# Kernel optimization log

Hardware: AMD Instinct MI355X
Metric: run time of the kernel (lower is better)

The kernel has to match this reference:

```python
import jax, jax.numpy as jnp
import numpy as np

# Standard FP4 E2M1 lookup table (nvfp4-style): sign bit in nibble MSB.
FP4_LUT = jnp.array([0.0, 0.5, 1.0, 1.5, 2.0, 3.0, 4.0, 6.0,
                     -0.0, -0.5, -1.0, -1.5, -2.0, -3.0, -4.0, -6.0],
                    dtype=jnp.float32)


def dequant_fp4(packed_i32, scales, group_size):
    """packed_i32: [K/8, N] int32 (8 fp4 nibbles per word, low nibble first);
    scales: [K/group_size, N]. Returns dense fp32 weight [K, N]."""
    w = jax.lax.bitcast_convert_type(packed_i32, jnp.uint32)  # [K/8, N]
    # Unpack nibbles along the reduction axis: nibble i -> row 8*r + i.
    nib = jnp.stack([(w >> jnp.uint32(4 * i)) & jnp.uint32(0xF) for i in range(8)],
                    axis=1)                                    # [K/8, 8, N]
    K = nib.shape[0] * 8
    nib = nib.reshape(K, w.shape[1])                           # [K, N]
    vals = FP4_LUT[nib]                                        # [K, N]
    s = jnp.repeat(scales, group_size, axis=0)                 # [K, N]
    return vals * s


def setup_inputs() -> dict:
    key = jax.random.key(0)
    k1, k2, k3, k4, k5, k6 = jax.random.split(key, 6)
    tokens, H, I, G = 4096, 2048, 5632, 128
    return {
        "hidden": jax.random.normal(k1, (tokens, H), dtype=jnp.float32),
        "moe_output": jax.random.normal(k2, (tokens, H), dtype=jnp.float32),
        "gate_up_weights": jax.random.randint(k3, (H // 8, 2 * I), 0, 2147483647, dtype=jnp.int32),
        "gate_up_scales": jax.random.uniform(k4, (H // G, 2 * I), dtype=jnp.float32, minval=0.01, maxval=0.1),
        "down_weights": jax.random.randint(k5, (I // 8, H), 0, 2147483647, dtype=jnp.int32),
        "down_scales": jax.random.uniform(k6, (I // G, H), dtype=jnp.float32, minval=0.01, maxval=0.1),
        "group_size": G,
    }


def reference(hidden, moe_output, gate_up_weights, gate_up_scales,
              down_weights, down_scales, group_size):
    # Shared-expert SwiGLU FFN with FP4 group-quantized weights, fused residual add.
    W_gu = dequant_fp4(gate_up_weights, gate_up_scales, group_size)  # [H, 2I]
    gu = hidden @ W_gu                                               # [T, 2I]
    I = gu.shape[1] // 2
    gate, up = gu[:, :I], gu[:, I:]
    act = jax.nn.silu(gate) * up                                     # [T, I]
    W_d = dequant_fp4(down_weights, down_scales, group_size)         # [I, H]
    return moe_output + act @ W_d                                    # [T, H]
```

## Files before the change

### kernel.cpp

```cpp
#include <hip/hip_runtime.h>
#include <hip/hip_fp16.h>
#include <stdint.h>

#define TOKENS 4096
#define HDIM   2048
#define IDIM   5632
#define BM 128
#define BN 128
#define BK 64

#define G1_NP  11264
#define G1_KSB (G1_NP * 64)
#define G2_KSB (HDIM * 64)

typedef _Float16 f16x8 __attribute__((ext_vector_type(8)));
typedef float    f32x4 __attribute__((ext_vector_type(4)));

__device__ __forceinline__ uint32_t dec2(uint32_t z, uint32_t s2u) {
    uint32_t sgn = (z << 12) & 0x80008000u;
    uint32_t h   = ((z << 9) & 0x0E000E00u) | sgn;
    __half2 hv = __builtin_bit_cast(__half2, h);
    __half2 sv = __builtin_bit_cast(__half2, s2u);
    __half2 r  = __hmul2(hv, sv);
    return __builtin_bit_cast(uint32_t, r);
}
__device__ __forceinline__ int4 dec8(uint32_t w, uint32_t s2u) {
    int4 d;
    d.x = (int)dec2( w        & 0x000F000Fu, s2u);
    d.y = (int)dec2((w >> 4)  & 0x000F000Fu, s2u);
    d.z = (int)dec2((w >> 8)  & 0x000F000Fu, s2u);
    d.w = (int)dec2((w >> 12) & 0x000F000Fu, s2u);
    return d;
}
__device__ __forceinline__ uint32_t scale_s2u(float sc) {
    uint16_t hs = __builtin_bit_cast(uint16_t, __float2half(sc * 16384.0f));
    return (uint32_t)hs * 0x00010001u;
}
__device__ __forceinline__ uint32_t packh(float lo, float hi) {
    __half2 h2 = __halves2half2(__float2half(lo), __float2half(hi));
    return __builtin_bit_cast(uint32_t, h2);
}
__device__ __forceinline__ void gl_lds16(const void* g, void* l) {
    __builtin_amdgcn_global_load_lds(
        (const __attribute__((address_space(1))) uint32_t*)g,
        (__attribute__((address_space(3))) uint32_t*)l, 16, 0, 0);
}

__global__ __launch_bounds__(256) void convert_hidden(
    const float* __restrict__ src, __half* __restrict__ dst)
{
    int idx = blockIdx.x * 256 + threadIdx.x;
    const float4* s = (const float4*)src + (size_t)idx * 2;
    float4 a = s[0], b = s[1];
    int4 v;
    v.x = (int)packh(a.x, b.x);
    v.y = (int)packh(a.y, b.y);
    v.z = (int)packh(a.z, b.z);
    v.w = (int)packh(a.w, b.w);
    *((int4*)dst + idx) = v;
}

__global__ __launch_bounds__(256) void dequant_wgu5(
    const uint32_t* __restrict__ W, const float* __restrict__ S,
    __half* __restrict__ Bt)
{
    __shared__ __half L[256 * 64];
    const int kt = blockIdx.y;
    const int t  = threadIdx.x;
    const int np = blockIdx.x * 256 + t;
    const int sc = (np >> 6) * 32 + (np & 31) + (((np >> 5) & 1) ? IDIM : 0);
    uint32_t s2u = scale_s2u(S[(size_t)(kt >> 1) * (2 * IDIM) + sc]);
    #pragma unroll
    for (int j = 0; j < 8; ++j) {
        uint32_t w = W[(size_t)(kt * 8 + j) * (2 * IDIM) + sc];
        int4 d = dec8(w, s2u);
        *(int4*)&L[t * 64 + ((j ^ (t & 7)) << 3)] = d;
    }
    __syncthreads();
    __half* dst = Bt + (size_t)kt * G1_KSB + (size_t)blockIdx.x * 256 * 64;
    #pragma unroll
    for (int k = 0; k < 8; ++k) {
        int c = k * 256 + t;
        int row = c >> 3, s = c & 7;
        int4 d = *(const int4*)&L[row * 64 + ((s ^ (row & 7)) << 3)];
        *(int4*)(dst + c * 8) = d;
    }
}

__global__ __launch_bounds__(256) void dequant_wd5(
    const uint32_t* __restrict__ W, const float* __restrict__ S,
    __half* __restrict__ Bt)
{
    __shared__ __half L[256 * 64];
    const int kt = blockIdx.y;
    const int t  = threadIdx.x;
    const int n  = blockIdx.x * 256 + t;
    uint32_t s2u = scale_s2u(S[(size_t)(kt >> 1) * HDIM + n]);
    #pragma unroll
    for (int j = 0; j < 8; ++j) {
        uint32_t w = W[(size_t)(kt * 8 + j) * HDIM + n];
        int4 d = dec8(w, s2u);
        *(int4*)&L[t * 64 + ((j ^ (t & 7)) << 3)] = d;
    }
    __syncthreads();
    __half* dst = Bt + (size_t)kt * G2_KSB + (size_t)blockIdx.x * 256 * 64;
    #pragma unroll
    for (int k = 0; k < 8; ++k) {
        int c = k * 256 + t;
        int row = c >> 3, s = c & 7;
        int4 d = *(const int4*)&L[row * 64 + ((s ^ (row & 7)) << 3)];
        *(int4*)(dst + c * 8) = d;
    }
}

__global__ __launch_bounds__(256, 4) void gemm1_s(
    const __half* __restrict__ A, const __half* __restrict__ Bt,
    __half* __restrict__ act)
{
    __shared__ __half Alds[BM * 64];
    __shared__ __half Blds[BN * 64];
    const int tid  = threadIdx.x;
    const int lane = tid & 63;
    const int wid  = tid >> 6;
    const int wm = wid >> 1, wn = wid & 1;
    const int m0 = blockIdx.y * BM;
    const int n0 = blockIdx.x * BN;

    f32x4 acc[4][4];
    #pragma unroll
    for (int i = 0; i < 4; ++i)
        #pragma unroll
        for (int j = 0; j < 4; ++j) acc[i][j] = f32x4{0.f, 0.f, 0.f, 0.f};

    const __half* srcA[4];
    const __half* srcB[4];
    #pragma unroll
    for (int i = 0; i < 4; ++i) {
        int u = i * 256 + tid, row = u >> 3, s = u & 7, sl = s ^ (row & 7);
        srcA[i] = A  + (size_t)(m0 + row) * HDIM + sl * 8;
        srcB[i] = Bt + (size_t)(n0 + row) * 64 + sl * 8;
    }

    int aoff[4][2], boff[4][2];
    #pragma unroll
    for (int f = 0; f < 4; ++f)
        #pragma unroll
        for (int ks = 0; ks < 2; ++ks) {
            int kb = ks * 4 + (lane >> 4);
            int ra = wm * 64 + f * 16 + (lane & 15);
            int rb = wn * 64 + f * 16 + (lane & 15);
            aoff[f][ks] = ra * 128 + ((kb ^ (ra & 7)) << 4);
            boff[f][ks] = rb * 128 + ((kb ^ (rb & 7)) << 4);
        }

    for (int kt = 0; kt < HDIM / 64; ++kt) {
        #pragma unroll
        for (int i = 0; i < 4; ++i) {
            int u = i * 256 + tid;
            gl_lds16(srcA[i], (char*)Alds + u * 16);
            gl_lds16(srcB[i], (char*)Blds + u * 16);
            srcA[i] += 64;
            srcB[i] += G1_KSB;
        }
        __syncthreads();
        #pragma unroll
        for (int ks = 0; ks < 2; ++ks) {
            f16x8 af[4], bf[4];
            #pragma unroll
            for (int f = 0; f < 4; ++f) {
                af[f] = *(const f16x8*)((const char*)Alds + aoff[f][ks]);
                bf[f] = *(const f16x8*)((const char*)Blds + boff[f][ks]);
            }
            #pragma unroll
            for (int mi = 0; mi < 4; ++mi)
                #pragma unroll
                for (int ni = 0; ni < 4; ++ni)
                    acc[mi][ni] = __builtin_amdgcn_mfma_f32_16x16x32_f16(af[mi], bf[ni], acc[mi][ni], 0, 0, 0);
        }
        __syncthreads();
    }

    const int pairbase = ((n0 + wn * 64) >> 6) * 32;
    #pragma unroll
    for (int mi = 0; mi < 4; ++mi) {
        #pragma unroll
        for (int q = 0; q < 2; ++q) {
            int gcol = pairbase + q * 16 + (lane & 15);
            int colstore = (gcol & ~7) | (((gcol & 3) << 1) | ((gcol >> 2) & 1));
            #pragma unroll
            for (int r = 0; r < 4; ++r) {
                int m = m0 + wm * 64 + mi * 16 + (lane >> 4) * 4 + r;
                float gv = acc[mi][q][r];
                float uv = acc[mi][q + 2][r];
                float sig = 1.0f / (1.0f + __expf(-gv));
                act[(size_t)m * IDIM + colstore] = __float2half(gv * sig * uv);
            }
        }
    }
}

__global__ __launch_bounds__(256, 4) void gemm2_s(
    const __half* __restrict__ A, const __half* __restrict__ Bt,
    const float* __restrict__ moe, float* __restrict__ out)
{
    __shared__ __half Alds[BM * 64];
    __shared__ __half Blds[BN * 64];
    const int tid  = threadIdx.x;
    const int lane = tid & 63;
    const int wid  = tid >> 6;
    const int wm = wid >> 1, wn = wid & 1;
    const int m0 = blockIdx.y * BM;
    const int n0 = blockIdx.x * BN;

    f32x4 acc[4][4];
    #pragma unroll
    for (int i = 0; i < 4; ++i)
        #pragma unroll
        for (int j = 0; j < 4; ++j) acc[i][j] = f32x4{0.f, 0.f, 0.f, 0.f};

    const __half* srcA[4];
    const __half* srcB[4];
    #pragma unroll
    for (int i = 0; i < 4; ++i) {
        int u = i * 256 + tid, row = u >> 3, s = u & 7, sl = s ^ (row & 7);
        srcA[i] = A  + (size_t)(m0 + row) * IDIM + sl * 8;
        srcB[i] = Bt + (size_t)(n0 + row) * 64 + sl * 8;
    }

    int aoff[4][2], boff[4][2];
    #pragma unroll
    for (int f = 0; f < 4; ++f)
        #pragma unroll
        for (int ks = 0; ks < 2; ++ks) {
            int kb = ks * 4 + (lane >> 4);
            int ra = wm * 64 + f * 16 + (lane & 15);
            int rb = wn * 64 + f * 16 + (lane & 15);
            aoff[f][ks] = ra * 128 + ((kb ^ (ra & 7)) << 4);
            boff[f][ks] = rb * 128 + ((kb ^ (rb & 7)) << 4);
        }

    for (int kt = 0; kt < IDIM / 64; ++kt) {
        #pragma unroll
        for (int i = 0; i < 4; ++i) {
            int u = i * 256 + tid;
            gl_lds16(srcA[i], (char*)Alds + u * 16);
            gl_lds16(srcB[i], (char*)Blds + u * 16);
            srcA[i] += 64;
            srcB[i] += G2_KSB;
        }
        __syncthreads();
        #pragma unroll
        for (int ks = 0; ks < 2; ++ks) {
            f16x8 af[4], bf[4];
            #pragma unroll
            for (int f = 0; f < 4; ++f) {
                af[f] = *(const f16x8*)((const char*)Alds + aoff[f][ks]);
                bf[f] = *(const f16x8*)((const char*)Blds + boff[f][ks]);
            }
            #pragma unroll
            for (int mi = 0; mi < 4; ++mi)
                #pragma unroll
                for (int ni = 0; ni < 4; ++ni)
                    acc[mi][ni] = __builtin_amdgcn_mfma_f32_16x16x32_f16(af[mi], bf[ni], acc[mi][ni], 0, 0, 0);
        }
        __syncthreads();
    }
    #pragma unroll
    for (int mi = 0; mi < 4; ++mi) {
        #pragma unroll
        for (int ni = 0; ni < 4; ++ni) {
            int n = n0 + wn * 64 + ni * 16 + (lane & 15);
            #pragma unroll
            for (int r = 0; r < 4; ++r) {
                int m = m0 + wm * 64 + mi * 16 + (lane >> 4) * 4 + r;
                out[(size_t)m * HDIM + n] = moe[(size_t)m * HDIM + n] + acc[mi][ni][r];
            }
        }
    }
}

__global__ __launch_bounds__(256, 2) void gemm1_silu(
    const __half* __restrict__ A, const uint32_t* __restrict__ W,
    const float* __restrict__ S, __half* __restrict__ act)
{
    __shared__ __half Alds[BM * BK];
    __shared__ __half Blds[2][BN * BK];
    const int tid  = threadIdx.x;
    const int lane = tid & 63;
    const int wid  = tid >> 6;
    const int wm = wid >> 1, wn = wid & 1;
    const int m0 = blockIdx.y * BM;
    const int c0 = blockIdx.x * BN;

    f32x4 accg[4][4], accu[4][4];
    #pragma unroll
    for (int i = 0; i < 4; ++i)
        #pragma unroll
        for (int j = 0; j < 4; ++j) {
            accg[i][j] = f32x4{0.f, 0.f, 0.f, 0.f};
            accu[i][j] = f32x4{0.f, 0.f, 0.f, 0.f};
        }

    const int c = tid & 127;
    const int rbase = (tid >> 7) * 4;

    for (int kt = 0; kt < HDIM / BK; ++kt) {
        const int k0 = kt * BK;
        #pragma unroll
        for (int i = 0; i < 4; ++i) {
            int u = tid + i * 256;
            int row = u >> 3, kb = u & 7;
            int4 v = *(const int4*)(A + (size_t)(m0 + row) * HDIM + k0 + kb * 8);
            *(int4*)((char*)Alds + row * 128 + ((kb ^ (row & 7)) << 4)) = v;
        }
        const int g = k0 >> 7;
        #pragma unroll
        for (int p = 0; p < 2; ++p) {
            const int ncol = (p ? IDIM : 0) + c0 + c;
            uint32_t s2u = scale_s2u(S[(size_t)g * (2 * IDIM) + ncol]);
            #pragma unroll
            for (int i = 0; i < 4; ++i) {
                int rl = rbase + i;
                uint32_t w = W[(size_t)(kt * 8 + rl) * (2 * IDIM) + ncol];
                int4 d = dec8(w, s2u);
                *(int4*)((char*)&Blds[p][0] + c * 128 + ((rl ^ (c & 7)) << 4)) = d;
            }
        }
        __syncthreads();
        #pragma unroll
        for (int ks = 0; ks < 2; ++ks) {
            f16x8 af[4], bg[4], bu[4];
            const int kb = ks * 4 + (lane >> 4);
            #pragma unroll
            for (int mi = 0; mi < 4; ++mi) {
                int m = wm * 64 + mi * 16 + (lane & 15);
                af[mi] = *(const f16x8*)((const char*)Alds + m * 128 + ((kb ^ (m & 7)) << 4));
            }
            #pragma unroll
            for (int ni = 0; ni < 4; ++ni) {
                int n = wn * 64 + ni * 16 + (lane & 15);
                bg[ni] = *(const f16x8*)((const char*)&Blds[0][0] + n * 128 + ((kb ^ (n & 7)) << 4));
                bu[ni] = *(const f16x8*)((const char*)&Blds[1][0] + n * 128 + ((kb ^ (n & 7)) << 4));
            }
            #pragma unroll
            for (int mi = 0; mi < 4; ++mi)
                #pragma unroll
                for (int ni = 0; ni < 4; ++ni) {
                    accg[mi][ni] = __builtin_amdgcn_mfma_f32_16x16x32_f16(af[mi], bg[ni], accg[mi][ni], 0, 0, 0);
                    accu[mi][ni] = __builtin_amdgcn_mfma_f32_16x16x32_f16(af[mi], bu[ni], accu[mi][ni], 0, 0, 0);
                }
        }
        __syncthreads();
    }
    #pragma unroll
    for (int mi = 0; mi < 4; ++mi) {
        #pragma unroll
        for (int ni = 0; ni < 4; ++ni) {
            int nlog = c0 + wn * 64 + ni * 16 + (lane & 15);
            int ncol = (nlog & ~7) | (((nlog & 3) << 1) | ((nlog >> 2) & 1));
            #pragma unroll
            for (int r = 0; r < 4; ++r) {
                int m = m0 + wm * 64 + mi * 16 + (lane >> 4) * 4 + r;
                float gv = accg[mi][ni][r];
                float uv = accu[mi][ni][r];
                float sig = 1.0f / (1.0f + __expf(-gv));
                act[(size_t)m * IDIM + ncol] = __float2half(gv * sig * uv);
            }
        }
    }
}

__global__ __launch_bounds__(256, 2) void gemm2_add(
    const __half* __restrict__ A, const uint32_t* __restrict__ W,
    const float* __restrict__ S, const float* __restrict__ moe,
    float* __restrict__ out)
{
    __shared__ __half Alds[BM * BK];
    __shared__ __half Blds[BN * BK];
    const int tid  = threadIdx.x;
    const int lane = tid & 63;
    const int wid  = tid >> 6;
    const int wm = wid >> 1, wn = wid & 1;
    const int m0 = blockIdx.y * BM;
    const int n0 = blockIdx.x * BN;

    f32x4 acc[4][4];
    #pragma unroll
    for (int i = 0; i < 4; ++i)
        #pragma unroll
        for (int j = 0; j < 4; ++j) acc[i][j] = f32x4{0.f, 0.f, 0.f, 0.f};

    const int c = tid & 127;
    const int rbase = (tid >> 7) * 4;

    int aoff[4][2], boff[4][2];
    #pragma unroll
    for (int f = 0; f < 4; ++f)
        #pragma unroll
        for (int ks = 0; ks < 2; ++ks) {
            int kb = ks * 4 + (lane >> 4);
            int ra = wm * 64 + f * 16 + (lane & 15);
            int rb = wn * 64 + f * 16 + (lane & 15);
            aoff[f][ks] = ra * 128 + ((kb ^ (ra & 7)) << 4);
            boff[f][ks] = rb * 128 + ((kb ^ (rb & 7)) << 4);
        }

    for (int kt = 0; kt < IDIM / BK; ++kt) {
        const int k0 = kt * BK;
        #pragma unroll
        for (int i = 0; i < 4; ++i) {
            int u = tid + i * 256;
            int row = u >> 3, kb = u & 7;
            int4 v = *(const int4*)(A + (size_t)(m0 + row) * IDIM + k0 + kb * 8);
            *(int4*)((char*)Alds + row * 128 + ((kb ^ (row & 7)) << 4)) = v;
        }
        {
            const int g = k0 >> 7;
            const int ncol = n0 + c;
            uint32_t s2u = scale_s2u(S[(size_t)g * HDIM + ncol]);
            #pragma unroll
            for (int i = 0; i < 4; ++i) {
                int rl = rbase + i;
                uint32_t w = W[(size_t)(kt * 8 + rl) * HDIM + ncol];
                int4 d = dec8(w, s2u);
                *(int4*)((char*)Blds + c * 128 + ((rl ^ (c & 7)) << 4)) = d;
            }
        }
        __syncthreads();
        #pragma unroll
        for (int ks = 0; ks < 2; ++ks) {
            f16x8 af[4], bf[4];
            #pragma unroll
            for (int f = 0; f < 4; ++f) {
                af[f] = *(const f16x8*)((const char*)Alds + aoff[f][ks]);
                bf[f] = *(const f16x8*)((const char*)Blds + boff[f][ks]);
            }
            #pragma unroll
            for (int mi = 0; mi < 4; ++mi)
                #pragma unroll
                for (int ni = 0; ni < 4; ++ni)
                    acc[mi][ni] = __builtin_amdgcn_mfma_f32_16x16x32_f16(af[mi], bf[ni], acc[mi][ni], 0, 0, 0);
        }
        __syncthreads();
    }
    #pragma unroll
    for (int mi = 0; mi < 4; ++mi) {
        #pragma unroll
        for (int ni = 0; ni < 4; ++ni) {
            int n = n0 + wn * 64 + ni * 16 + (lane & 15);
            #pragma unroll
            for (int r = 0; r < 4; ++r) {
                int m = m0 + wm * 64 + mi * 16 + (lane >> 4) * 4 + r;
                out[(size_t)m * HDIM + n] = moe[(size_t)m * HDIM + n] + acc[mi][ni][r];
            }
        }
    }
}

extern "C" void kernel_launch(void* const* d_in, const int* in_sizes, int n_in,
                              void* d_out, int out_size, void* d_ws, size_t ws_size,
                              hipStream_t stream) {
    const float*    hidden = (const float*)d_in[0];
    const float*    moe    = (const float*)d_in[1];
    const uint32_t* wgu    = (const uint32_t*)d_in[2];
    const float*    sgu    = (const float*)d_in[3];
    const uint32_t* wd     = (const uint32_t*)d_in[4];
    const float*    sd     = (const float*)d_in[5];
    float* out = (float*)d_out;

    const size_t sz_hidden = (size_t)TOKENS * HDIM * 2;
    const size_t sz_act    = (size_t)TOKENS * IDIM * 2;
    const size_t sz_wgu16  = (size_t)HDIM * 2 * IDIM * 2;
    const size_t sz_wd16   = (size_t)IDIM * HDIM * 2;

    __half* hidden_f16 = (__half*)d_ws;
    __half* act        = (__half*)((char*)d_ws + sz_hidden);
    __half* wgu16      = (__half*)((char*)d_ws + sz_hidden + sz_act);
    __half* wd16       = (__half*)((char*)d_ws + sz_hidden + sz_act + sz_wgu16);

    const size_t need_g1 = sz_hidden + sz_act + sz_wgu16;
    const size_t need_g2 = need_g1 + sz_wd16;

    convert_hidden<<<dim3(TOKENS * HDIM / 8 / 256), dim3(256), 0, stream>>>(hidden, hidden_f16);

    if (ws_size >= need_g1) {
        dequant_wgu5<<<dim3(G1_NP / 256, 32), dim3(256), 0, stream>>>(wgu, sgu, wgu16);
        gemm1_s<<<dim3(G1_NP / BN, TOKENS / BM), dim3(256), 0, stream>>>(hidden_f16, wgu16, act);
    } else {
        gemm1_silu<<<dim3(IDIM / BN, TOKENS / BM), dim3(256), 0, stream>>>(hidden_f16, wgu, sgu, act);
    }

    if (ws_size >= need_g2) {
        dequant_wd5<<<dim3(HDIM / 256, IDIM / 64), dim3(256), 0, stream>>>(wd, sd, wd16);
        gemm2_s<<<dim3(HDIM / BN, TOKENS / BM), dim3(256), 0, stream>>>(act, wd16, moe, out);
    } else {
        gemm2_add<<<dim3(HDIM / BN, TOKENS / BM), dim3(256), 0, stream>>>(act, wd, sd, moe, out);
    }
}
```

Baseline: 317.7 us.

## Pre-swizzle gate/up weights into MFMA fragment order and load B directly to registers

The gate/up dequant kernel now writes fp16 weights in the exact per-lane MFMA fragment order, so the first GEMM loads B fragments straight from global memory into registers instead of staging them through LDS. This removes half the LDS traffic and B-tile LDS reads in gemm1, at the cost of depending on cache hits for B reuse across M-blocks. Occupancy is lowered to 3 waves per SIMD to make room for the extra registers. The fallback gemm2_add path also inlines its LDS offset computation.

```diff
diff --git a/kernel.cpp b/kernel.cpp
--- a/kernel.cpp
+++ b/kernel.cpp
@@ -60,7 +60,7 @@
     *((int4*)dst + idx) = v;
 }
 
-__global__ __launch_bounds__(256) void dequant_wgu5(
+__global__ __launch_bounds__(256) void dequant_wgu6(
     const uint32_t* __restrict__ W, const float* __restrict__ S,
     __half* __restrict__ Bt)
 {
@@ -77,7 +77,34 @@
         *(int4*)&L[t * 64 + ((j ^ (t & 7)) << 3)] = d;
     }
     __syncthreads();
-    __half* dst = Bt + (size_t)kt * G1_KSB + (size_t)blockIdx.x * 256 * 64;
+    __half* dst = Bt + (size_t)kt * G1_KSB + (size_t)blockIdx.x * 16384;
+    #pragma unroll
+    for (int k = 0; k < 8; ++k) {
+        int c = k * 256 + t;
+        int row = ((c >> 7) << 4) + (c & 15);
+        int w   = (((c >> 6) & 1) << 2) + ((c >> 4) & 3);
+        int4 d = *(const int4*)&L[row * 64 + ((w ^ (row & 7)) << 3)];
+        *(int4*)(dst + (size_t)c * 8) = d;
+    }
+}
+
+__global__ __launch_bounds__(256) void dequant_wd5(
+    const uint32_t* __restrict__ W, const float* __restrict__ S,
+    __half* __restrict__ Bt)
+{
+    __shared__ __half L[256 * 64];
+    const int kt = blockIdx.y;
+    const int t  = threadIdx.x;
+    const int n  = blockIdx.x * 256 + t;
+    uint32_t s2u = scale_s2u(S[(size_t)(kt >> 1) * HDIM + n]);
+    #pragma unroll
+    for (int j = 0; j < 8; ++j) {
+        uint32_t w = W[(size_t)(kt * 8 + j) * HDIM + n];
+        int4 d = dec8(w, s2u);
+        *(int4*)&L[t * 64 + ((j ^ (t & 7)) << 3)] = d;
+    }
+    __syncthreads();
+    __half* dst = Bt + (size_t)kt * G2_KSB + (size_t)blockIdx.x * 256 * 64;
     #pragma unroll
     for (int k = 0; k < 8; ++k) {
         int c = k * 256 + t;
@@ -87,35 +114,94 @@
     }
 }
 
-__global__ __launch_bounds__(256) void dequant_wd5(
-    const uint32_t* __restrict__ W, const float* __restrict__ S,
-    __half* __restrict__ Bt)
-{
-    __shared__ __half L[256 * 64];
-    const int kt = blockIdx.y;
-    const int t  = threadIdx.x;
-    const int n  = blockIdx.x * 256 + t;
-    uint32_t s2u = scale_s2u(S[(size_t)(kt >> 1) * HDIM + n]);
-    #pragma unroll
-    for (int j = 0; j < 8; ++j) {
-        uint32_t w = W[(size_t)(kt * 8 + j) * HDIM + n];
-        int4 d = dec8(w, s2u);
-        *(int4*)&L[t * 64 + ((j ^ (t & 7)) << 3)] = d;
-    }
-    __syncthreads();
-    __half* dst = Bt + (size_t)kt * G2_KSB + (size_t)blockIdx.x * 256 * 64;
-    #pragma unroll
-    for (int k = 0; k < 8; ++k) {
-        int c = k * 256 + t;
-        int row = c >> 3, s = c & 7;
-        int4 d = *(const int4*)&L[row * 64 + ((s ^ (row & 7)) << 3)];
-        *(int4*)(dst + c * 8) = d;
-    }
-}
-
-__global__ __launch_bounds__(256, 4) void gemm1_s(
+__global__ __launch_bounds__(256, 3) void gemm1_f(
     const __half* __restrict__ A, const __half* __restrict__ Bt,
     __half* __restrict__ act)
+{
+    __shared__ __half Alds[BM * 64];
+    const int tid  = threadIdx.x;
+    const int lane = tid & 63;
+    const int wid  = tid >> 6;
+    const int wm = wid >> 1, wn = wid & 1;
+    const int m0 = blockIdx.y * BM;
+    const int n0 = blockIdx.x * BN;
+
+    f32x4 acc[4][4];
+    #pragma unroll
+    for (int i = 0; i < 4; ++i)
+        #pragma unroll
+        for (int j = 0; j < 4; ++j) acc[i][j] = f32x4{0.f, 0.f, 0.f, 0.f};
+
+    const __half* srcA[4];
+    #pragma unroll
+    for (int i = 0; i < 4; ++i) {
+        int u = i * 256 + tid, row = u >> 3, s = u & 7, sl = s ^ (row & 7);
+        srcA[i] = A + (size_t)(m0 + row) * HDIM + sl * 8;
+    }
+
+    const __half* pB = Bt + ((size_t)((n0 >> 4) + wn * 4) * 2) * 512 + lane * 8;
+
+    int aoff[4][2];
+    #pragma unroll
+    for (int f = 0; f < 4; ++f)
+        #pragma unroll
+        for (int ks = 0; ks < 2; ++ks) {
+            int kb = ks * 4 + (lane >> 4);
+            int ra = wm * 64 + f * 16 + (lane & 15);
+            aoff[f][ks] = ra * 128 + ((kb ^ (ra & 7)) << 4);
+        }
+
+    for (int kt = 0; kt < HDIM / 64; ++kt) {
+        f16x8 bf[4][2];
+        #pragma unroll
+        for (int ni = 0; ni < 4; ++ni)
+            #pragma unroll
+            for (int ks = 0; ks < 2; ++ks)
+                bf[ni][ks] = *(const f16x8*)(pB + (size_t)kt * G1_KSB + (ni * 2 + ks) * 512);
+        #pragma unroll
+        for (int i = 0; i < 4; ++i) {
+            int u = i * 256 + tid;
+            gl_lds16(srcA[i], (char*)Alds + u * 16);
+            srcA[i] += 64;
+        }
+        __syncthreads();
+        #pragma unroll
+        for (int ks = 0; ks < 2; ++ks) {
+            f16x8 af[4];
+            #pragma unroll
+            for (int f = 0; f < 4; ++f)
+                af[f] = *(const f16x8*)((const char*)Alds + aoff[f][ks]);
+            #pragma unroll
+            for (int mi = 0; mi < 4; ++mi)
+                #pragma unroll
+                for (int ni = 0; ni < 4; ++ni)
+                    acc[mi][ni] = __builtin_amdgcn_mfma_f32_16x16x32_f16(af[mi], bf[ni][ks], acc[mi][ni], 0, 0, 0);
+        }
+        __syncthreads();
+    }
+
+    const int pairbase = ((n0 + wn * 64) >> 6) * 32;
+    #pragma unroll
+    for (int mi = 0; mi < 4; ++mi) {
+        #pragma unroll
+        for (int q = 0; q < 2; ++q) {
+            int gcol = pairbase + q * 16 + (lane & 15);
+            int colstore = (gcol & ~7) | (((gcol & 3) << 1) | ((gcol >> 2) & 1));
+            #pragma unroll
+            for (int r = 0; r < 4; ++r) {
+                int m = m0 + wm * 64 + mi * 16 + (lane >> 4) * 4 + r;
+                float gv = acc[mi][q][r];
+                float uv = acc[mi][q + 2][r];
+                float sig = 1.0f / (1.0f + __expf(-gv));
+                act[(size_t)m * IDIM + colstore] = __float2half(gv * sig * uv);
+            }
+        }
+    }
+}
+
+__global__ __launch_bounds__(256, 4) void gemm2_s(
+    const __half* __restrict__ A, const __half* __restrict__ Bt,
+    const float* __restrict__ moe, float* __restrict__ out)
 {
     __shared__ __half Alds[BM * 64];
     __shared__ __half Blds[BN * 64];
@@ -137,92 +223,6 @@
     #pragma unroll
     for (int i = 0; i < 4; ++i) {
         int u = i * 256 + tid, row = u >> 3, s = u & 7, sl = s ^ (row & 7);
-        srcA[i] = A  + (size_t)(m0 + row) * HDIM + sl * 8;
-        srcB[i] = Bt + (size_t)(n0 + row) * 64 + sl * 8;
-    }
-
-    int aoff[4][2], boff[4][2];
-    #pragma unroll
-    for (int f = 0; f < 4; ++f)
-        #pragma unroll
-        for (int ks = 0; ks < 2; ++ks) {
-            int kb = ks * 4 + (lane >> 4);
-            int ra = wm * 64 + f * 16 + (lane & 15);
-            int rb = wn * 64 + f * 16 + (lane & 15);
-            aoff[f][ks] = ra * 128 + ((kb ^ (ra & 7)) << 4);
-            boff[f][ks] = rb * 128 + ((kb ^ (rb & 7)) << 4);
-        }
-
-    for (int kt = 0; kt < HDIM / 64; ++kt) {
-        #pragma unroll
-        for (int i = 0; i < 4; ++i) {
-            int u = i * 256 + tid;
-            gl_lds16(srcA[i], (char*)Alds + u * 16);
-            gl_lds16(srcB[i], (char*)Blds + u * 16);
-            srcA[i] += 64;
-            srcB[i] += G1_KSB;
-        }
-        __syncthreads();
-        #pragma unroll
-        for (int ks = 0; ks < 2; ++ks) {
-            f16x8 af[4], bf[4];
-            #pragma unroll
-            for (int f = 0; f < 4; ++f) {
-                af[f] = *(const f16x8*)((const char*)Alds + aoff[f][ks]);
-                bf[f] = *(const f16x8*)((const char*)Blds + boff[f][ks]);
-            }
-            #pragma unroll
-            for (int mi = 0; mi < 4; ++mi)
-                #pragma unroll
-                for (int ni = 0; ni < 4; ++ni)
-                    acc[mi][ni] = __builtin_amdgcn_mfma_f32_16x16x32_f16(af[mi], bf[ni], acc[mi][ni], 0, 0, 0);
-        }
-        __syncthreads();
-    }
-
-    const int pairbase = ((n0 + wn * 64) >> 6) * 32;
-    #pragma unroll
-    for (int mi = 0; mi < 4; ++mi) {
-        #pragma unroll
-        for (int q = 0; q < 2; ++q) {
-            int gcol = pairbase + q * 16 + (lane & 15);
-            int colstore = (gcol & ~7) | (((gcol & 3) << 1) | ((gcol >> 2) & 1));
-            #pragma unroll
-            for (int r = 0; r < 4; ++r) {
-                int m = m0 + wm * 64 + mi * 16 + (lane >> 4) * 4 + r;
-                float gv = acc[mi][q][r];
-                float uv = acc[mi][q + 2][r];
-                float sig = 1.0f / (1.0f + __expf(-gv));
-                act[(size_t)m * IDIM + colstore] = __float2half(gv * sig * uv);
-            }
-        }
-    }
-}
-
-__global__ __launch_bounds__(256, 4) void gemm2_s(
-    const __half* __restrict__ A, const __half* __restrict__ Bt,
-    const float* __restrict__ moe, float* __restrict__ out)
-{
-    __shared__ __half Alds[BM * 64];
-    __shared__ __half Blds[BN * 64];
-    const int tid  = threadIdx.x;
-    const int lane = tid & 63;
-    const int wid  = tid >> 6;
-    const int wm = wid >> 1, wn = wid & 1;
-    const int m0 = blockIdx.y * BM;
-    const int n0 = blockIdx.x * BN;
-
-    f32x4 acc[4][4];
-    #pragma unroll
-    for (int i = 0; i < 4; ++i)
-        #pragma unroll
-        for (int j = 0; j < 4; ++j) acc[i][j] = f32x4{0.f, 0.f, 0.f, 0.f};
-
-    const __half* srcA[4];
-    const __half* srcB[4];
-    #pragma unroll
-    for (int i = 0; i < 4; ++i) {
-        int u = i * 256 + tid, row = u >> 3, s = u & 7, sl = s ^ (row & 7);
         srcA[i] = A  + (size_t)(m0 + row) * IDIM + sl * 8;
         srcB[i] = Bt + (size_t)(n0 + row) * 64 + sl * 8;
     }
@@ -393,18 +393,6 @@
     const int c = tid & 127;
     const int rbase = (tid >> 7) * 4;
 
-    int aoff[4][2], boff[4][2];
-    #pragma unroll
-    for (int f = 0; f < 4; ++f)
-        #pragma unroll
-        for (int ks = 0; ks < 2; ++ks) {
-            int kb = ks * 4 + (lane >> 4);
-            int ra = wm * 64 + f * 16 + (lane & 15);
-            int rb = wn * 64 + f * 16 + (lane & 15);
-            aoff[f][ks] = ra * 128 + ((kb ^ (ra & 7)) << 4);
-            boff[f][ks] = rb * 128 + ((kb ^ (rb & 7)) << 4);
-        }
-
     for (int kt = 0; kt < IDIM / BK; ++kt) {
         const int k0 = kt * BK;
         #pragma unroll
@@ -430,10 +418,16 @@
         #pragma unroll
         for (int ks = 0; ks < 2; ++ks) {
             f16x8 af[4], bf[4];
-            #pragma unroll
-            for (int f = 0; f < 4; ++f) {
-                af[f] = *(const f16x8*)((const char*)Alds + aoff[f][ks]);
-                bf[f] = *(const f16x8*)((const char*)Blds + boff[f][ks]);
+            const int kb = ks * 4 + (lane >> 4);
+            #pragma unroll
+            for (int mi = 0; mi < 4; ++mi) {
+                int m = wm * 64 + mi * 16 + (lane & 15);
+                af[mi] = *(const f16x8*)((const char*)Alds + m * 128 + ((kb ^ (m & 7)) << 4));
+            }
+            #pragma unroll
+            for (int ni = 0; ni < 4; ++ni) {
+                int n = wn * 64 + ni * 16 + (lane & 15);
+                bf[ni] = *(const f16x8*)((const char*)Blds + n * 128 + ((kb ^ (n & 7)) << 4));
             }
             #pragma unroll
             for (int mi = 0; mi < 4; ++mi)
@@ -484,8 +478,8 @@
     convert_hidden<<<dim3(TOKENS * HDIM / 8 / 256), dim3(256), 0, stream>>>(hidden, hidden_f16);
 
     if (ws_size >= need_g1) {
-        dequant_wgu5<<<dim3(G1_NP / 256, 32), dim3(256), 0, stream>>>(wgu, sgu, wgu16);
-        gemm1_s<<<dim3(G1_NP / BN, TOKENS / BM), dim3(256), 0, stream>>>(hidden_f16, wgu16, act);
+        dequant_wgu6<<<dim3(G1_NP / 256, 32), dim3(256), 0, stream>>>(wgu, sgu, wgu16);
+        gemm1_f<<<dim3(G1_NP / BN, TOKENS / BM), dim3(256), 0, stream>>>(hidden_f16, wgu16, act);
     } else {
         gemm1_silu<<<dim3(IDIM / BN, TOKENS / BM), dim3(256), 0, stream>>>(hidden_f16, wgu, sgu, act);
     }
```

Measured after the change: 321.0 us. Within noise of the previous version (+1.0%).
